# Performance work log

Measured on AMD Instinct MI355X. Metric: run time of the kernel, lower is better.

## Reference

```python
import jax, jax.numpy as jnp
import numpy as np

N_OBJ, N_REG = 4096, 8192
D_HO = D_HR = 512
GATE_W = 128
E = 131072


def setup_inputs() -> dict:
    key = jax.random.key(0)
    ks = jax.random.split(key, 10)
    s = 1.0 / np.sqrt(D_HO + D_HR)
    return {
        "feature_obj": jax.random.normal(ks[0], (N_OBJ, D_HO), jnp.float32),
        "feature_region": jax.random.normal(ks[1], (N_REG, D_HR), jnp.float32),
        # edge lists (tgt, src) equivalent to np.where(select_mat > 0)
        "r2o_tgt": jnp.sort(jax.random.randint(ks[2], (E,), 0, N_OBJ, jnp.int32)),
        "r2o_src": jax.random.randint(ks[3], (E,), 0, N_REG, jnp.int32),
        "o2r_tgt": jnp.sort(jax.random.randint(ks[4], (E,), 0, N_REG, jnp.int32)),
        "o2r_src": jax.random.randint(ks[5], (E,), 0, N_OBJ, jnp.int32),
        # attention gate Linear(dim_src+dim_tgt -> gate_width), bias=True
        "gw_r2o": jax.random.uniform(ks[6], (GATE_W, D_HR + D_HO), jnp.float32, -s, s),
        "gb_r2o": jnp.zeros((GATE_W,), jnp.float32),
        "gw_o2r": jax.random.uniform(ks[7], (GATE_W, D_HO + D_HR), jnp.float32, -s, s),
        "gb_o2r": jnp.zeros((GATE_W,), jnp.float32),
        # transform Sequential(ReLU, Linear(dim -> dim, bias=True))
        "tw_r2o": jax.random.uniform(ks[8], (D_HO, D_HR), jnp.float32, -s, s),
        "tb_r2o": jnp.zeros((D_HO,), jnp.float32),
        "tw_o2r": jax.random.uniform(ks[9], (D_HR, D_HO), jnp.float32, -s, s),
        "tb_o2r": jnp.zeros((D_HR,), jnp.float32),
    }


def _message(tgt_feat, src_feat, tgt_idx, src_idx, gw, gb, num_tgt):
    # gather per-edge source/target features: [E, ds], [E, dt]
    src = src_feat[src_idx]
    tgt = tgt_feat[tgt_idx]
    # Attention_Module: gate = mean(sigmoid(W @ relu(cat(src, tgt)) + b))
    g = jax.nn.relu(jnp.concatenate([src, tgt], axis=-1))
    gate = jnp.mean(jax.nn.sigmoid(g @ gw.T + gb), axis=-1, keepdims=True)  # [E, 1]
    msg = src * gate
    agg = jax.ops.segment_sum(msg, tgt_idx, num_segments=num_tgt)
    # mps_use_average=True -> per-target mean; targets with no edges stay zero
    cnt = jax.ops.segment_sum(jnp.ones((tgt_idx.shape[0], 1), msg.dtype), tgt_idx, num_segments=num_tgt)
    return agg / jnp.maximum(cnt, 1.0)


def reference(feature_obj, feature_region, r2o_tgt, r2o_src, o2r_tgt, o2r_src,
              gw_r2o, gb_r2o, gw_o2r, gb_o2r, tw_r2o, tb_r2o, tw_o2r, tb_o2r):
    m_r2o = _message(feature_obj, feature_region, r2o_tgt, r2o_src, gw_r2o, gb_r2o, N_OBJ)
    out_obj = feature_obj + jax.nn.relu(m_r2o) @ tw_r2o.T + tb_r2o
    m_o2r = _message(feature_region, feature_obj, o2r_tgt, o2r_src, gw_o2r, gb_o2r, N_REG)
    out_reg = feature_region + jax.nn.relu(m_o2r) @ tw_o2r.T + tb_o2r
    return (out_obj, out_reg)
```

## Files before the change

kernel.cpp:

```cpp
#include <hip/hip_runtime.h>

constexpr int N_OBJ = 4096, N_REG = 8192, D = 512, GW = 128, NE = 131072;

typedef __attribute__((ext_vector_type(8))) short short8;
typedef __attribute__((ext_vector_type(4))) float f32x4;
typedef __attribute__((ext_vector_type(2))) float f32x2;

__device__ inline short f2bf(float f) {
  unsigned u = __builtin_bit_cast(unsigned, f);
  unsigned r = (u + 0x7FFF + ((u >> 16) & 1)) >> 16;
  return (short)r;
}

__global__ __launch_bounds__(256) void cast_csr(
    const float* __restrict__ feat_reg, const float* __restrict__ feat_obj,
    const float* __restrict__ gw_r2o, const float* __restrict__ gw_o2r,
    const float* __restrict__ tw_r2o, const float* __restrict__ tw_o2r,
    const int* __restrict__ t_r2o, const int* __restrict__ t_o2r,
    unsigned char* __restrict__ raw_reg, short* __restrict__ relu_reg,
    unsigned char* __restrict__ raw_obj, short* __restrict__ relu_obj,
    short* __restrict__ Wreg, short* __restrict__ Wobj,
    short* __restrict__ btw_r2o, short* __restrict__ btw_o2r,
    int* __restrict__ off_r2o, int* __restrict__ off_o2r) {
  int i = blockIdx.x * 256 + threadIdx.x;
  if (i >= 1769472) {
    i -= 1769472;
    const int* tgt; int* off; int t;
    if (i <= N_OBJ) { tgt = t_r2o; off = off_r2o; t = i; }
    else {
      i -= N_OBJ + 1;
      if (i > N_REG) return;
      tgt = t_o2r; off = off_o2r; t = i;
    }
    int lo = 0, hi = NE;
    while (lo < hi) {
      int mid = (lo + hi) >> 1;
      if (tgt[mid] < t) lo = mid + 1; else hi = mid;
    }
    off[t] = lo;
    return;
  }
  if (i < 1572864) {
    const float* src; unsigned char* draw; short* drelu; int j = i;
    if (j < 1048576) { src = feat_reg; draw = raw_reg; drelu = relu_reg; }
    else { j -= 1048576; src = feat_obj; draw = raw_obj; drelu = relu_obj; }
    float4 v = ((const float4*)src)[j];
    int p = __builtin_amdgcn_cvt_pk_fp8_f32(v.x, v.y, 0, false);
    p = __builtin_amdgcn_cvt_pk_fp8_f32(v.z, v.w, p, true);
    ((unsigned*)draw)[j] = (unsigned)p;
    ((short4*)drelu)[j] = make_short4(f2bf(fmaxf(v.x, 0.f)), f2bf(fmaxf(v.y, 0.f)),
                                      f2bf(fmaxf(v.z, 0.f)), f2bf(fmaxf(v.w, 0.f)));
    return;
  }
  i -= 1572864;
  const float* src; short* dst; int di;
  if (i < 32768) {
    int row = i >> 7, c4 = i & 127;
    src = (row < 128) ? gw_r2o + (size_t)row * 1024 + c4 * 4
                      : gw_o2r + (size_t)(row - 128) * 1024 + 512 + c4 * 4;
    dst = Wreg; di = i;
  } else if (i < 65536) {
    int k = i - 32768, row = k >> 7, c4 = k & 127;
    src = (row < 128) ? gw_r2o + (size_t)row * 1024 + 512 + c4 * 4
                      : gw_o2r + (size_t)(row - 128) * 1024 + c4 * 4;
    dst = Wobj; di = k;
  } else if (i < 131072) { di = i - 65536; src = tw_r2o + (size_t)di * 4; dst = btw_r2o; }
  else                   { di = i - 131072; src = tw_o2r + (size_t)di * 4; dst = btw_o2r; }
  float4 v = *(const float4*)src;
  ((short4*)dst)[di] = make_short4(f2bf(v.x), f2bf(v.y), f2bf(v.z), f2bf(v.w));
}

struct GemmPair {
  const short* A[2]; const short* B[2];
  const float* res[2]; const float* bias[2];
  void* C[2];
  int nb0;
  int nxb;
  int ldc;
};

template<bool EPI, int BN>
__global__ __launch_bounds__(256) void gemm_pair(GemmPair gp) {
  constexpr int NF = BN / 32;
  __shared__ short As[2][128 * 32];
  __shared__ short Bs[2][BN * 32];
  int b = blockIdx.x;
  const int pi = (b >= gp.nb0) ? 1 : 0;
  if (pi) b -= gp.nb0;
  const int bx = b % gp.nxb, by = b / gp.nxb;
  const short* __restrict__ A = gp.A[pi];
  const short* __restrict__ B = gp.B[pi];
  const int ldc = gp.ldc;
  const int tid = threadIdx.x;
  const int lane = tid & 63, w = tid >> 6;
  const int m0 = by * 128, n0 = bx * BN;
  const int wm = (w >> 1) * 64, wn = (w & 1) * (BN / 2);
  const int sr = lane >> 2, sc = (lane & 3) * 8;
  const int fr = lane & 15, fk = (lane >> 4) * 8;

  f32x4 acc[4][NF];
#pragma unroll
  for (int i = 0; i < 4; ++i)
#pragma unroll
    for (int j = 0; j < NF; ++j) acc[i][j] = (f32x4){0.f, 0.f, 0.f, 0.f};

  auto stage = [&](int buf, int k0) {
#pragma unroll
    for (int h = 0; h < 2; ++h) {
      int rg = w * 32 + h * 16;
      const short* ga = A + (size_t)(m0 + rg + sr) * 512 + k0 + sc;
      __builtin_amdgcn_global_load_lds(
          (const __attribute__((address_space(1))) void*)ga,
          (__attribute__((address_space(3))) void*)&As[buf][rg * 32], 16, 0, 0);
    }
#pragma unroll
    for (int h = 0; h < BN / 64; ++h) {
      int rg = w * (BN / 4) + h * 16;
      const short* gb = B + (size_t)(n0 + rg + sr) * 512 + k0 + sc;
      __builtin_amdgcn_global_load_lds(
          (const __attribute__((address_space(1))) void*)gb,
          (__attribute__((address_space(3))) void*)&Bs[buf][rg * 32], 16, 0, 0);
    }
  };
  auto compute = [&](int buf) {
    short8 a[4], bb[NF];
#pragma unroll
    for (int i = 0; i < 4; ++i)
      a[i] = *(const short8*)&As[buf][(wm + i * 16 + fr) * 32 + fk];
#pragma unroll
    for (int j = 0; j < NF; ++j)
      bb[j] = *(const short8*)&Bs[buf][(wn + j * 16 + fr) * 32 + fk];
#pragma unroll
    for (int i = 0; i < 4; ++i)
#pragma unroll
      for (int j = 0; j < NF; ++j)
        acc[i][j] = __builtin_amdgcn_mfma_f32_16x16x32_bf16(a[i], bb[j], acc[i][j], 0, 0, 0);
  };

  stage(0, 0);
  __syncthreads();
  int cur = 0;
  for (int k0 = 0; k0 < 512 - 32; k0 += 32) {
    stage(cur ^ 1, k0 + 32);
    compute(cur);
    __syncthreads();
    cur ^= 1;
  }
  compute(cur);

  if (EPI) {
    float* C = (float*)gp.C[pi];
    const float* res = gp.res[pi];
    const float* bias = gp.bias[pi];
#pragma unroll
    for (int i = 0; i < 4; ++i)
#pragma unroll
      for (int j = 0; j < NF; ++j) {
        int n = n0 + wn + j * 16 + fr;
#pragma unroll
        for (int r = 0; r < 4; ++r) {
          int m = m0 + wm + i * 16 + (lane >> 4) * 4 + r;
          C[(size_t)m * ldc + n] = acc[i][j][r] + res[(size_t)m * ldc + n] + bias[n];
        }
      }
  } else {
    unsigned char* C = (unsigned char*)gp.C[pi];
#pragma unroll
    for (int i = 0; i < 4; ++i)
#pragma unroll
      for (int j = 0; j < NF; ++j) {
        int n = n0 + wn + j * 16 + fr;
#pragma unroll
        for (int r = 0; r < 4; ++r) {
          int m = m0 + wm + i * 16 + (lane >> 4) * 4 + r;
          int pk = __builtin_amdgcn_cvt_pk_fp8_f32(acc[i][j][r], acc[i][j][r], 0, false);
          C[(size_t)m * ldc + n] = (unsigned char)(pk & 0xFF);
        }
      }
  }
}

__global__ __launch_bounds__(256) void fused_msg(
    const unsigned char* __restrict__ Preg, const unsigned char* __restrict__ Pobj,
    const unsigned char* __restrict__ raw_reg, const unsigned char* __restrict__ raw_obj,
    const int* __restrict__ r2o_src, const int* __restrict__ o2r_src,
    const int* __restrict__ off_r2o, const int* __restrict__ off_o2r,
    const float* __restrict__ gb_r2o, const float* __restrict__ gb_o2r,
    short* __restrict__ m_obj, short* __restrict__ m_reg) {
  __shared__ float red[4][512];
  int t = blockIdx.x;
  const unsigned char *PA, *PB, *feat; const int *src, *off; const float* gb;
  short* mo; int po;
  if (t < N_OBJ) {
    PA = Preg; PB = Pobj; feat = raw_reg; src = r2o_src; off = off_r2o;
    gb = gb_r2o; mo = m_obj; po = 0;
  } else {
    t -= N_OBJ;
    PA = Pobj; PB = Preg; feat = raw_obj; src = o2r_src; off = off_o2r;
    gb = gb_o2r; mo = m_reg; po = 128;
  }
  const int tid = threadIdx.x, lane = tid & 63, w = tid >> 6;
  const int hw = lane >> 5, l = lane & 31;
  const int e0 = off[t], e1 = off[t + 1];
  unsigned pbu = *(const unsigned*)&PB[(size_t)t * 256 + po + l * 4];
  f32x2 pb01 = __builtin_amdgcn_cvt_pk_f32_fp8((int)pbu, false);
  f32x2 pb23 = __builtin_amdgcn_cvt_pk_f32_fp8((int)pbu, true);
  float4 gbv = *(const float4*)&gb[l * 4];
  const float c0 = pb01.x + gbv.x, c1 = pb01.y + gbv.y;
  const float c2 = pb23.x + gbv.z, c3 = pb23.y + gbv.w;
  float acc[16] = {};

  auto sig4 = [&](unsigned pau) -> float {
    f32x2 a01 = __builtin_amdgcn_cvt_pk_f32_fp8((int)pau, false);
    f32x2 a23 = __builtin_amdgcn_cvt_pk_f32_fp8((int)pau, true);
    return __builtin_amdgcn_rcpf(1.f + __expf(-(a01.x + c0)))
         + __builtin_amdgcn_rcpf(1.f + __expf(-(a01.y + c1)))
         + __builtin_amdgcn_rcpf(1.f + __expf(-(a23.x + c2)))
         + __builtin_amdgcn_rcpf(1.f + __expf(-(a23.y + c3)));
  };
  auto accum = [&](uint4 fv, float gs) {
    f32x2 f0 = __builtin_amdgcn_cvt_pk_f32_fp8((int)fv.x, false);
    f32x2 f1 = __builtin_amdgcn_cvt_pk_f32_fp8((int)fv.x, true);
    f32x2 f2 = __builtin_amdgcn_cvt_pk_f32_fp8((int)fv.y, false);
    f32x2 f3 = __builtin_amdgcn_cvt_pk_f32_fp8((int)fv.y, true);
    f32x2 f4 = __builtin_amdgcn_cvt_pk_f32_fp8((int)fv.z, false);
    f32x2 f5 = __builtin_amdgcn_cvt_pk_f32_fp8((int)fv.z, true);
    f32x2 f6 = __builtin_amdgcn_cvt_pk_f32_fp8((int)fv.w, false);
    f32x2 f7 = __builtin_amdgcn_cvt_pk_f32_fp8((int)fv.w, true);
    acc[0]  += f0.x * gs; acc[1]  += f0.y * gs;
    acc[2]  += f1.x * gs; acc[3]  += f1.y * gs;
    acc[4]  += f2.x * gs; acc[5]  += f2.y * gs;
    acc[6]  += f3.x * gs; acc[7]  += f3.y * gs;
    acc[8]  += f4.x * gs; acc[9]  += f4.y * gs;
    acc[10] += f5.x * gs; acc[11] += f5.y * gs;
    acc[12] += f6.x * gs; acc[13] += f6.y * gs;
    acc[14] += f7.x * gs; acc[15] += f7.y * gs;
  };

  int e = e0 + w * 2 + hw;
  for (; e + 8 < e1; e += 16) {
    int s0 = src[e], s1 = src[e + 8];
    unsigned pau0 = *(const unsigned*)&PA[(size_t)s0 * 256 + po + l * 4];
    uint4 fv0 = *(const uint4*)&feat[(size_t)s0 * 512 + l * 16];
    unsigned pau1 = *(const unsigned*)&PA[(size_t)s1 * 256 + po + l * 4];
    uint4 fv1 = *(const uint4*)&feat[(size_t)s1 * 512 + l * 16];
    float gs0 = sig4(pau0), gs1 = sig4(pau1);
#pragma unroll
    for (int msk = 16; msk >= 1; msk >>= 1) {
      gs0 += __shfl_xor(gs0, msk, 64);
      gs1 += __shfl_xor(gs1, msk, 64);
    }
    accum(fv0, gs0);
    accum(fv1, gs1);
  }
  for (; e < e1; e += 8) {
    int s = src[e];
    unsigned pau = *(const unsigned*)&PA[(size_t)s * 256 + po + l * 4];
    uint4 fv = *(const uint4*)&feat[(size_t)s * 512 + l * 16];
    float gs = sig4(pau);
#pragma unroll
    for (int msk = 16; msk >= 1; msk >>= 1) gs += __shfl_xor(gs, msk, 64);
    accum(fv, gs);
  }
#pragma unroll
  for (int jj = 0; jj < 16; ++jj) acc[jj] += __shfl_xor(acc[jj], 32, 64);
  if (hw == 0) {
#pragma unroll
    for (int q = 0; q < 4; ++q)
      *(float4*)&red[w][l * 16 + q * 4] =
          (float4){acc[q * 4], acc[q * 4 + 1], acc[q * 4 + 2], acc[q * 4 + 3]};
  }
  __syncthreads();
  const float inv = (1.0f / 128.0f) / fmaxf((float)(e1 - e0), 1.0f);
  const int d = tid * 2;
  float s0 = red[0][d] + red[1][d] + red[2][d] + red[3][d];
  float s1 = red[0][d + 1] + red[1][d + 1] + red[2][d + 1] + red[3][d + 1];
  short2 o;
  o.x = f2bf(fmaxf(s0 * inv, 0.f));
  o.y = f2bf(fmaxf(s1 * inv, 0.f));
  *(short2*)(mo + (size_t)t * 512 + d) = o;
}

extern "C" void kernel_launch(void* const* d_in, const int* in_sizes, int n_in,
                              void* d_out, int out_size, void* d_ws, size_t ws_size,
                              hipStream_t stream) {
  const float* feat_obj = (const float*)d_in[0];
  const float* feat_reg = (const float*)d_in[1];
  const int*   r2o_tgt  = (const int*)d_in[2];
  const int*   r2o_src  = (const int*)d_in[3];
  const int*   o2r_tgt  = (const int*)d_in[4];
  const int*   o2r_src  = (const int*)d_in[5];
  const float* gw_r2o   = (const float*)d_in[6];
  const float* gb_r2o   = (const float*)d_in[7];
  const float* gw_o2r   = (const float*)d_in[8];
  const float* gb_o2r   = (const float*)d_in[9];
  const float* tw_r2o   = (const float*)d_in[10];
  const float* tb_r2o   = (const float*)d_in[11];
  const float* tw_o2r   = (const float*)d_in[12];
  const float* tb_o2r   = (const float*)d_in[13];
  float* out_obj = (float*)d_out;
  float* out_reg = out_obj + (size_t)N_OBJ * D;

  size_t cur = 0;
  auto alloc = [&](size_t bytes) -> void* {
    cur = (cur + 255) & ~(size_t)255;
    void* p = (char*)d_ws + cur;
    cur += bytes;
    return p;
  };
  int*   off_r2o = (int*)alloc((N_OBJ + 1) * sizeof(int));
  int*   off_o2r = (int*)alloc((N_REG + 1) * sizeof(int));
  unsigned char* raw_reg = (unsigned char*)alloc((size_t)N_REG * D);
  unsigned char* raw_obj = (unsigned char*)alloc((size_t)N_OBJ * D);
  short* relu_reg= (short*)alloc((size_t)N_REG * D * 2);
  short* relu_obj= (short*)alloc((size_t)N_OBJ * D * 2);
  short* Wreg    = (short*)alloc((size_t)256 * D * 2);
  short* Wobj    = (short*)alloc((size_t)256 * D * 2);
  short* btw_r2o = (short*)alloc((size_t)D * D * 2);
  short* btw_o2r = (short*)alloc((size_t)D * D * 2);
  unsigned char* Preg = (unsigned char*)alloc((size_t)N_REG * 256);
  unsigned char* Pobj = (unsigned char*)alloc((size_t)N_OBJ * 256);
  short* m_obj   = (short*)alloc((size_t)N_OBJ * D * 2);
  short* m_reg   = (short*)alloc((size_t)N_REG * D * 2);

  cast_csr<<<6961, 256, 0, stream>>>(feat_reg, feat_obj, gw_r2o, gw_o2r, tw_r2o, tw_o2r,
                                     r2o_tgt, o2r_tgt,
                                     raw_reg, relu_reg, raw_obj, relu_obj,
                                     Wreg, Wobj, btw_r2o, btw_o2r, off_r2o, off_o2r);

  GemmPair proj;
  proj.A[0] = relu_reg; proj.B[0] = Wreg; proj.C[0] = Preg;
  proj.A[1] = relu_obj; proj.B[1] = Wobj; proj.C[1] = Pobj;
  proj.res[0] = proj.res[1] = nullptr; proj.bias[0] = proj.bias[1] = nullptr;
  proj.nb0 = 4 * (N_REG / 128); proj.nxb = 4; proj.ldc = 256;
  gemm_pair<false, 64><<<384, 256, 0, stream>>>(proj);

  fused_msg<<<N_OBJ + N_REG, 256, 0, stream>>>(Preg, Pobj, raw_reg, raw_obj,
                                               r2o_src, o2r_src, off_r2o, off_o2r,
                                               gb_r2o, gb_o2r, m_obj, m_reg);

  GemmPair tr;
  tr.A[0] = m_reg; tr.B[0] = btw_o2r; tr.res[0] = feat_reg; tr.bias[0] = tb_o2r; tr.C[0] = out_reg;
  tr.A[1] = m_obj; tr.B[1] = btw_r2o; tr.res[1] = feat_obj; tr.bias[1] = tb_r2o; tr.C[1] = out_obj;
  tr.nb0 = 4 * (N_REG / 128); tr.nxb = 4; tr.ldc = D;
  gemm_pair<true, 128><<<384, 256, 0, stream>>>(tr);
}
```

Before: 188.6 us.

## Map one wavefront per target node in fused message kernel, drop LDS reduction

Reworks fused_msg so that each 64-lane wavefront owns one target node instead of a 256-thread block per node. Lanes are split into four quarter-wave groups of 16, each handling one edge at a time with 8 gate columns and 32 feature bytes per lane. The per-block shared-memory reduction and __syncthreads are replaced by cross-quarter shuffles, and the output is written as a single 16-byte store per lane. This cuts block count and sync overhead, at the cost of more registers per lane (32 accumulators) and less edge-level parallelism per target, since only 4 edges are in flight per node instead of 8.

```diff
diff --git a/kernel.cpp b/kernel.cpp
--- a/kernel.cpp
+++ b/kernel.cpp
@@ -187,8 +187,9 @@
     const int* __restrict__ off_r2o, const int* __restrict__ off_o2r,
     const float* __restrict__ gb_r2o, const float* __restrict__ gb_o2r,
     short* __restrict__ m_obj, short* __restrict__ m_reg) {
-  __shared__ float red[4][512];
-  int t = blockIdx.x;
+  const int tid = threadIdx.x, w = tid >> 6, lane = tid & 63;
+  const int q = lane >> 4, l = lane & 15;
+  int t = blockIdx.x * 4 + w;
   const unsigned char *PA, *PB, *feat; const int *src, *off; const float* gb;
   short* mo; int po;
   if (t < N_OBJ) {
@@ -199,86 +200,60 @@
     PA = Pobj; PB = Preg; feat = raw_obj; src = o2r_src; off = off_o2r;
     gb = gb_o2r; mo = m_reg; po = 128;
   }
-  const int tid = threadIdx.x, lane = tid & 63, w = tid >> 6;
-  const int hw = lane >> 5, l = lane & 31;
   const int e0 = off[t], e1 = off[t + 1];
-  unsigned pbu = *(const unsigned*)&PB[(size_t)t * 256 + po + l * 4];
-  f32x2 pb01 = __builtin_amdgcn_cvt_pk_f32_fp8((int)pbu, false);
-  f32x2 pb23 = __builtin_amdgcn_cvt_pk_f32_fp8((int)pbu, true);
-  float4 gbv = *(const float4*)&gb[l * 4];
-  const float c0 = pb01.x + gbv.x, c1 = pb01.y + gbv.y;
-  const float c2 = pb23.x + gbv.z, c3 = pb23.y + gbv.w;
-  float acc[16] = {};
-
-  auto sig4 = [&](unsigned pau) -> float {
-    f32x2 a01 = __builtin_amdgcn_cvt_pk_f32_fp8((int)pau, false);
-    f32x2 a23 = __builtin_amdgcn_cvt_pk_f32_fp8((int)pau, true);
-    return __builtin_amdgcn_rcpf(1.f + __expf(-(a01.x + c0)))
-         + __builtin_amdgcn_rcpf(1.f + __expf(-(a01.y + c1)))
-         + __builtin_amdgcn_rcpf(1.f + __expf(-(a23.x + c2)))
-         + __builtin_amdgcn_rcpf(1.f + __expf(-(a23.y + c3)));
-  };
-  auto accum = [&](uint4 fv, float gs) {
-    f32x2 f0 = __builtin_amdgcn_cvt_pk_f32_fp8((int)fv.x, false);
-    f32x2 f1 = __builtin_amdgcn_cvt_pk_f32_fp8((int)fv.x, true);
-    f32x2 f2 = __builtin_amdgcn_cvt_pk_f32_fp8((int)fv.y, false);
-    f32x2 f3 = __builtin_amdgcn_cvt_pk_f32_fp8((int)fv.y, true);
-    f32x2 f4 = __builtin_amdgcn_cvt_pk_f32_fp8((int)fv.z, false);
-    f32x2 f5 = __builtin_amdgcn_cvt_pk_f32_fp8((int)fv.z, true);
-    f32x2 f6 = __builtin_amdgcn_cvt_pk_f32_fp8((int)fv.w, false);
-    f32x2 f7 = __builtin_amdgcn_cvt_pk_f32_fp8((int)fv.w, true);
-    acc[0]  += f0.x * gs; acc[1]  += f0.y * gs;
-    acc[2]  += f1.x * gs; acc[3]  += f1.y * gs;
-    acc[4]  += f2.x * gs; acc[5]  += f2.y * gs;
-    acc[6]  += f3.x * gs; acc[7]  += f3.y * gs;
-    acc[8]  += f4.x * gs; acc[9]  += f4.y * gs;
-    acc[10] += f5.x * gs; acc[11] += f5.y * gs;
-    acc[12] += f6.x * gs; acc[13] += f6.y * gs;
-    acc[14] += f7.x * gs; acc[15] += f7.y * gs;
-  };
-
-  int e = e0 + w * 2 + hw;
-  for (; e + 8 < e1; e += 16) {
-    int s0 = src[e], s1 = src[e + 8];
-    unsigned pau0 = *(const unsigned*)&PA[(size_t)s0 * 256 + po + l * 4];
-    uint4 fv0 = *(const uint4*)&feat[(size_t)s0 * 512 + l * 16];
-    unsigned pau1 = *(const unsigned*)&PA[(size_t)s1 * 256 + po + l * 4];
-    uint4 fv1 = *(const uint4*)&feat[(size_t)s1 * 512 + l * 16];
-    float gs0 = sig4(pau0), gs1 = sig4(pau1);
-#pragma unroll
-    for (int msk = 16; msk >= 1; msk >>= 1) {
-      gs0 += __shfl_xor(gs0, msk, 64);
-      gs1 += __shfl_xor(gs1, msk, 64);
-    }
-    accum(fv0, gs0);
-    accum(fv1, gs1);
-  }
-  for (; e < e1; e += 8) {
+  uint2 pbu = *(const uint2*)&PB[(size_t)t * 256 + po + l * 8];
+  f32x2 pb0 = __builtin_amdgcn_cvt_pk_f32_fp8((int)pbu.x, false);
+  f32x2 pb1 = __builtin_amdgcn_cvt_pk_f32_fp8((int)pbu.x, true);
+  f32x2 pb2 = __builtin_amdgcn_cvt_pk_f32_fp8((int)pbu.y, false);
+  f32x2 pb3 = __builtin_amdgcn_cvt_pk_f32_fp8((int)pbu.y, true);
+  float4 gA = *(const float4*)&gb[l * 8];
+  float4 gB = *(const float4*)&gb[l * 8 + 4];
+  const float c0 = pb0.x + gA.x, c1 = pb0.y + gA.y;
+  const float c2 = pb1.x + gA.z, c3 = pb1.y + gA.w;
+  const float c4 = pb2.x + gB.x, c5 = pb2.y + gB.y;
+  const float c6 = pb3.x + gB.z, c7 = pb3.y + gB.w;
+
+  float acc[32] = {};
+  for (int e = e0 + q; e < e1; e += 4) {
     int s = src[e];
-    unsigned pau = *(const unsigned*)&PA[(size_t)s * 256 + po + l * 4];
-    uint4 fv = *(const uint4*)&feat[(size_t)s * 512 + l * 16];
-    float gs = sig4(pau);
-#pragma unroll
-    for (int msk = 16; msk >= 1; msk >>= 1) gs += __shfl_xor(gs, msk, 64);
-    accum(fv, gs);
-  }
-#pragma unroll
-  for (int jj = 0; jj < 16; ++jj) acc[jj] += __shfl_xor(acc[jj], 32, 64);
-  if (hw == 0) {
-#pragma unroll
-    for (int q = 0; q < 4; ++q)
-      *(float4*)&red[w][l * 16 + q * 4] =
-          (float4){acc[q * 4], acc[q * 4 + 1], acc[q * 4 + 2], acc[q * 4 + 3]};
-  }
-  __syncthreads();
+    uint2 pau = *(const uint2*)&PA[(size_t)s * 256 + po + l * 8];
+    uint4 f0 = *(const uint4*)&feat[(size_t)s * 512 + l * 32];
+    uint4 f1 = *(const uint4*)&feat[(size_t)s * 512 + l * 32 + 16];
+    f32x2 a0 = __builtin_amdgcn_cvt_pk_f32_fp8((int)pau.x, false);
+    f32x2 a1 = __builtin_amdgcn_cvt_pk_f32_fp8((int)pau.x, true);
+    f32x2 a2 = __builtin_amdgcn_cvt_pk_f32_fp8((int)pau.y, false);
+    f32x2 a3 = __builtin_amdgcn_cvt_pk_f32_fp8((int)pau.y, true);
+    float gs = __builtin_amdgcn_rcpf(1.f + __expf(-(a0.x + c0)))
+             + __builtin_amdgcn_rcpf(1.f + __expf(-(a0.y + c1)))
+             + __builtin_amdgcn_rcpf(1.f + __expf(-(a1.x + c2)))
+             + __builtin_amdgcn_rcpf(1.f + __expf(-(a1.y + c3)))
+             + __builtin_amdgcn_rcpf(1.f + __expf(-(a2.x + c4)))
+             + __builtin_amdgcn_rcpf(1.f + __expf(-(a2.y + c5)))
+             + __builtin_amdgcn_rcpf(1.f + __expf(-(a3.x + c6)))
+             + __builtin_amdgcn_rcpf(1.f + __expf(-(a3.y + c7)));
+#pragma unroll
+    for (int msk = 8; msk >= 1; msk >>= 1) gs += __shfl_xor(gs, msk, 64);
+    unsigned fd[8] = {f0.x, f0.y, f0.z, f0.w, f1.x, f1.y, f1.z, f1.w};
+#pragma unroll
+    for (int d = 0; d < 8; ++d) {
+      f32x2 lo = __builtin_amdgcn_cvt_pk_f32_fp8((int)fd[d], false);
+      f32x2 hi = __builtin_amdgcn_cvt_pk_f32_fp8((int)fd[d], true);
+      acc[d * 4 + 0] += lo.x * gs;
+      acc[d * 4 + 1] += lo.y * gs;
+      acc[d * 4 + 2] += hi.x * gs;
+      acc[d * 4 + 3] += hi.y * gs;
+    }
+  }
+#pragma unroll
+  for (int j = 0; j < 32; ++j) {
+    acc[j] += __shfl_xor(acc[j], 16, 64);
+    acc[j] += __shfl_xor(acc[j], 32, 64);
+  }
   const float inv = (1.0f / 128.0f) / fmaxf((float)(e1 - e0), 1.0f);
-  const int d = tid * 2;
-  float s0 = red[0][d] + red[1][d] + red[2][d] + red[3][d];
-  float s1 = red[0][d + 1] + red[1][d + 1] + red[2][d + 1] + red[3][d + 1];
-  short2 o;
-  o.x = f2bf(fmaxf(s0 * inv, 0.f));
-  o.y = f2bf(fmaxf(s1 * inv, 0.f));
-  *(short2*)(mo + (size_t)t * 512 + d) = o;
+  short8 o;
+#pragma unroll
+  for (int k = 0; k < 8; ++k) o[k] = f2bf(fmaxf(acc[q * 8 + k] * inv, 0.f));
+  *(short8*)(mo + (size_t)t * 512 + l * 32 + q * 8) = o;
 }
 
 extern "C" void kernel_launch(void* const* d_in, const int* in_sizes, int n_in,
@@ -335,9 +310,9 @@
   proj.nb0 = 4 * (N_REG / 128); proj.nxb = 4; proj.ldc = 256;
   gemm_pair<false, 64><<<384, 256, 0, stream>>>(proj);
 
-  fused_msg<<<N_OBJ + N_REG, 256, 0, stream>>>(Preg, Pobj, raw_reg, raw_obj,
-                                               r2o_src, o2r_src, off_r2o, off_o2r,
-                                               gb_r2o, gb_o2r, m_obj, m_reg);
+  fused_msg<<<(N_OBJ + N_REG) / 4, 256, 0, stream>>>(Preg, Pobj, raw_reg, raw_obj,
+                                                     r2o_src, o2r_src, off_r2o, off_o2r,
+                                                     gb_r2o, gb_o2r, m_obj, m_reg);
 
   GemmPair tr;
   tr.A[0] = m_reg; tr.B[0] = btw_o2r; tr.res[0] = feat_reg; tr.bias[0] = tb_o2r; tr.C[0] = out_reg;
```

New measurement: 193.3 us. 1.02x slower.

## Interleave per-node gate projection and fp8 features into one gathered record

Applied to the files above, without the earlier changes.

Packs each source node's 128-byte fp8 gate projection next to its 512-byte fp8 features in a 640-byte record, so each edge gather reads one contiguous record instead of two separate arrays. The projection GEMM epilogue now splits its output columns between these records and a separate compact target-side projection array. The message kernel's two-edge unrolled loop is also dropped in favour of a simple single-edge loop, which may reduce memory-level parallelism per wave.

```diff
diff --git a/kernel.cpp b/kernel.cpp
--- a/kernel.cpp
+++ b/kernel.cpp
@@ -1,6 +1,7 @@
 #include <hip/hip_runtime.h>
 
 constexpr int N_OBJ = 4096, N_REG = 8192, D = 512, GW = 128, NE = 131072;
+constexpr int REC = 640;
 
 typedef __attribute__((ext_vector_type(8))) short short8;
 typedef __attribute__((ext_vector_type(4))) float f32x4;
@@ -17,8 +18,8 @@
     const float* __restrict__ gw_r2o, const float* __restrict__ gw_o2r,
     const float* __restrict__ tw_r2o, const float* __restrict__ tw_o2r,
     const int* __restrict__ t_r2o, const int* __restrict__ t_o2r,
-    unsigned char* __restrict__ raw_reg, short* __restrict__ relu_reg,
-    unsigned char* __restrict__ raw_obj, short* __restrict__ relu_obj,
+    unsigned char* __restrict__ comb_reg, short* __restrict__ relu_reg,
+    unsigned char* __restrict__ comb_obj, short* __restrict__ relu_obj,
     short* __restrict__ Wreg, short* __restrict__ Wobj,
     short* __restrict__ btw_r2o, short* __restrict__ btw_o2r,
     int* __restrict__ off_r2o, int* __restrict__ off_o2r) {
@@ -41,13 +42,14 @@
     return;
   }
   if (i < 1572864) {
-    const float* src; unsigned char* draw; short* drelu; int j = i;
-    if (j < 1048576) { src = feat_reg; draw = raw_reg; drelu = relu_reg; }
-    else { j -= 1048576; src = feat_obj; draw = raw_obj; drelu = relu_obj; }
+    const float* src; unsigned char* comb; short* drelu; int j = i;
+    if (j < 1048576) { src = feat_reg; comb = comb_reg; drelu = relu_reg; }
+    else { j -= 1048576; src = feat_obj; comb = comb_obj; drelu = relu_obj; }
     float4 v = ((const float4*)src)[j];
     int p = __builtin_amdgcn_cvt_pk_fp8_f32(v.x, v.y, 0, false);
     p = __builtin_amdgcn_cvt_pk_fp8_f32(v.z, v.w, p, true);
-    ((unsigned*)draw)[j] = (unsigned)p;
+    int row = j >> 7, c4 = j & 127;
+    *(unsigned*)&comb[(size_t)row * REC + 128 + c4 * 4] = (unsigned)p;
     ((short4*)drelu)[j] = make_short4(f2bf(fmaxf(v.x, 0.f)), f2bf(fmaxf(v.y, 0.f)),
                                       f2bf(fmaxf(v.z, 0.f)), f2bf(fmaxf(v.w, 0.f)));
     return;
@@ -74,9 +76,9 @@
   const short* A[2]; const short* B[2];
   const float* res[2]; const float* bias[2];
   void* C[2];
-  int nb0;
-  int nxb;
-  int ldc;
+  void* Clo[2]; void* Chi[2];
+  int lo_stride[2]; int hi_stride[2];
+  int nb0, nxb, ldc;
 };
 
 template<bool EPI, int BN>
@@ -90,7 +92,6 @@
   const int bx = b % gp.nxb, by = b / gp.nxb;
   const short* __restrict__ A = gp.A[pi];
   const short* __restrict__ B = gp.B[pi];
-  const int ldc = gp.ldc;
   const int tid = threadIdx.x;
   const int lane = tid & 63, w = tid >> 6;
   const int m0 = by * 128, n0 = bx * BN;
@@ -152,6 +153,7 @@
     float* C = (float*)gp.C[pi];
     const float* res = gp.res[pi];
     const float* bias = gp.bias[pi];
+    const int ldc = gp.ldc;
 #pragma unroll
     for (int i = 0; i < 4; ++i)
 #pragma unroll
@@ -164,7 +166,9 @@
         }
       }
   } else {
-    unsigned char* C = (unsigned char*)gp.C[pi];
+    unsigned char* Clo = (unsigned char*)gp.Clo[pi];
+    unsigned char* Chi = (unsigned char*)gp.Chi[pi];
+    const int ls = gp.lo_stride[pi], hs = gp.hi_stride[pi];
 #pragma unroll
     for (int i = 0; i < 4; ++i)
 #pragma unroll
@@ -174,35 +178,36 @@
         for (int r = 0; r < 4; ++r) {
           int m = m0 + wm + i * 16 + (lane >> 4) * 4 + r;
           int pk = __builtin_amdgcn_cvt_pk_fp8_f32(acc[i][j][r], acc[i][j][r], 0, false);
-          C[(size_t)m * ldc + n] = (unsigned char)(pk & 0xFF);
+          unsigned char v = (unsigned char)(pk & 0xFF);
+          if (n < 128) Clo[(size_t)m * ls + n] = v;
+          else         Chi[(size_t)m * hs + (n - 128)] = v;
         }
       }
   }
 }
 
 __global__ __launch_bounds__(256) void fused_msg(
-    const unsigned char* __restrict__ Preg, const unsigned char* __restrict__ Pobj,
-    const unsigned char* __restrict__ raw_reg, const unsigned char* __restrict__ raw_obj,
+    const unsigned char* __restrict__ comb_reg, const unsigned char* __restrict__ comb_obj,
+    const unsigned char* __restrict__ PB_r2o, const unsigned char* __restrict__ PB_o2r,
     const int* __restrict__ r2o_src, const int* __restrict__ o2r_src,
     const int* __restrict__ off_r2o, const int* __restrict__ off_o2r,
     const float* __restrict__ gb_r2o, const float* __restrict__ gb_o2r,
     short* __restrict__ m_obj, short* __restrict__ m_reg) {
   __shared__ float red[4][512];
   int t = blockIdx.x;
-  const unsigned char *PA, *PB, *feat; const int *src, *off; const float* gb;
-  short* mo; int po;
+  const unsigned char *recs, *PBp; const int *src, *off; const float* gb; short* mo;
   if (t < N_OBJ) {
-    PA = Preg; PB = Pobj; feat = raw_reg; src = r2o_src; off = off_r2o;
-    gb = gb_r2o; mo = m_obj; po = 0;
+    recs = comb_reg; PBp = PB_r2o; src = r2o_src; off = off_r2o;
+    gb = gb_r2o; mo = m_obj;
   } else {
     t -= N_OBJ;
-    PA = Pobj; PB = Preg; feat = raw_obj; src = o2r_src; off = off_o2r;
-    gb = gb_o2r; mo = m_reg; po = 128;
+    recs = comb_obj; PBp = PB_o2r; src = o2r_src; off = off_o2r;
+    gb = gb_o2r; mo = m_reg;
   }
   const int tid = threadIdx.x, lane = tid & 63, w = tid >> 6;
   const int hw = lane >> 5, l = lane & 31;
   const int e0 = off[t], e1 = off[t + 1];
-  unsigned pbu = *(const unsigned*)&PB[(size_t)t * 256 + po + l * 4];
+  unsigned pbu = *(const unsigned*)&PBp[(size_t)t * 128 + l * 4];
   f32x2 pb01 = __builtin_amdgcn_cvt_pk_f32_fp8((int)pbu, false);
   f32x2 pb23 = __builtin_amdgcn_cvt_pk_f32_fp8((int)pbu, true);
   float4 gbv = *(const float4*)&gb[l * 4];
@@ -210,57 +215,29 @@
   const float c2 = pb23.x + gbv.z, c3 = pb23.y + gbv.w;
   float acc[16] = {};
 
-  auto sig4 = [&](unsigned pau) -> float {
+  for (int e = e0 + w * 2 + hw; e < e1; e += 8) {
+    int s = src[e];
+    const unsigned char* rec = recs + (size_t)s * REC;
+    unsigned pau = *(const unsigned*)&rec[l * 4];
+    uint4 fv = *(const uint4*)&rec[128 + l * 16];
     f32x2 a01 = __builtin_amdgcn_cvt_pk_f32_fp8((int)pau, false);
     f32x2 a23 = __builtin_amdgcn_cvt_pk_f32_fp8((int)pau, true);
-    return __builtin_amdgcn_rcpf(1.f + __expf(-(a01.x + c0)))
-         + __builtin_amdgcn_rcpf(1.f + __expf(-(a01.y + c1)))
-         + __builtin_amdgcn_rcpf(1.f + __expf(-(a23.x + c2)))
-         + __builtin_amdgcn_rcpf(1.f + __expf(-(a23.y + c3)));
-  };
-  auto accum = [&](uint4 fv, float gs) {
-    f32x2 f0 = __builtin_amdgcn_cvt_pk_f32_fp8((int)fv.x, false);
-    f32x2 f1 = __builtin_amdgcn_cvt_pk_f32_fp8((int)fv.x, true);
-    f32x2 f2 = __builtin_amdgcn_cvt_pk_f32_fp8((int)fv.y, false);
-    f32x2 f3 = __builtin_amdgcn_cvt_pk_f32_fp8((int)fv.y, true);
-    f32x2 f4 = __builtin_amdgcn_cvt_pk_f32_fp8((int)fv.z, false);
-    f32x2 f5 = __builtin_amdgcn_cvt_pk_f32_fp8((int)fv.z, true);
-    f32x2 f6 = __builtin_amdgcn_cvt_pk_f32_fp8((int)fv.w, false);
-    f32x2 f7 = __builtin_amdgcn_cvt_pk_f32_fp8((int)fv.w, true);
-    acc[0]  += f0.x * gs; acc[1]  += f0.y * gs;
-    acc[2]  += f1.x * gs; acc[3]  += f1.y * gs;
-    acc[4]  += f2.x * gs; acc[5]  += f2.y * gs;
-    acc[6]  += f3.x * gs; acc[7]  += f3.y * gs;
-    acc[8]  += f4.x * gs; acc[9]  += f4.y * gs;
-    acc[10] += f5.x * gs; acc[11] += f5.y * gs;
-    acc[12] += f6.x * gs; acc[13] += f6.y * gs;
-    acc[14] += f7.x * gs; acc[15] += f7.y * gs;
-  };
-
-  int e = e0 + w * 2 + hw;
-  for (; e + 8 < e1; e += 16) {
-    int s0 = src[e], s1 = src[e + 8];
-    unsigned pau0 = *(const unsigned*)&PA[(size_t)s0 * 256 + po + l * 4];
-    uint4 fv0 = *(const uint4*)&feat[(size_t)s0 * 512 + l * 16];
-    unsigned pau1 = *(const unsigned*)&PA[(size_t)s1 * 256 + po + l * 4];
-    uint4 fv1 = *(const uint4*)&feat[(size_t)s1 * 512 + l * 16];
-    float gs0 = sig4(pau0), gs1 = sig4(pau1);
-#pragma unroll
-    for (int msk = 16; msk >= 1; msk >>= 1) {
-      gs0 += __shfl_xor(gs0, msk, 64);
-      gs1 += __shfl_xor(gs1, msk, 64);
-    }
-    accum(fv0, gs0);
-    accum(fv1, gs1);
-  }
-  for (; e < e1; e += 8) {
-    int s = src[e];
-    unsigned pau = *(const unsigned*)&PA[(size_t)s * 256 + po + l * 4];
-    uint4 fv = *(const uint4*)&feat[(size_t)s * 512 + l * 16];
-    float gs = sig4(pau);
+    float gs = __builtin_amdgcn_rcpf(1.f + __expf(-(a01.x + c0)))
+             + __builtin_amdgcn_rcpf(1.f + __expf(-(a01.y + c1)))
+             + __builtin_amdgcn_rcpf(1.f + __expf(-(a23.x + c2)))
+             + __builtin_amdgcn_rcpf(1.f + __expf(-(a23.y + c3)));
 #pragma unroll
     for (int msk = 16; msk >= 1; msk >>= 1) gs += __shfl_xor(gs, msk, 64);
-    accum(fv, gs);
+    unsigned fd[4] = {fv.x, fv.y, fv.z, fv.w};
+#pragma unroll
+    for (int d = 0; d < 4; ++d) {
+      f32x2 lo = __builtin_amdgcn_cvt_pk_f32_fp8((int)fd[d], false);
+      f32x2 hi = __builtin_amdgcn_cvt_pk_f32_fp8((int)fd[d], true);
+      acc[d * 4 + 0] += lo.x * gs;
+      acc[d * 4 + 1] += lo.y * gs;
+      acc[d * 4 + 2] += hi.x * gs;
+      acc[d * 4 + 3] += hi.y * gs;
+    }
   }
 #pragma unroll
   for (int jj = 0; jj < 16; ++jj) acc[jj] += __shfl_xor(acc[jj], 32, 64);
@@ -310,38 +287,45 @@
   };
   int*   off_r2o = (int*)alloc((N_OBJ + 1) * sizeof(int));
   int*   off_o2r = (int*)alloc((N_REG + 1) * sizeof(int));
-  unsigned char* raw_reg = (unsigned char*)alloc((size_t)N_REG * D);
-  unsigned char* raw_obj = (unsigned char*)alloc((size_t)N_OBJ * D);
+  unsigned char* comb_reg = (unsigned char*)alloc((size_t)N_REG * REC);
+  unsigned char* comb_obj = (unsigned char*)alloc((size_t)N_OBJ * REC);
+  unsigned char* PB_r2o   = (unsigned char*)alloc((size_t)N_OBJ * 128);
+  unsigned char* PB_o2r   = (unsigned char*)alloc((size_t)N_REG * 128);
   short* relu_reg= (short*)alloc((size_t)N_REG * D * 2);
   short* relu_obj= (short*)alloc((size_t)N_OBJ * D * 2);
   short* Wreg    = (short*)alloc((size_t)256 * D * 2);
   short* Wobj    = (short*)alloc((size_t)256 * D * 2);
   short* btw_r2o = (short*)alloc((size_t)D * D * 2);
   short* btw_o2r = (short*)alloc((size_t)D * D * 2);
-  unsigned char* Preg = (unsigned char*)alloc((size_t)N_REG * 256);
-  unsigned char* Pobj = (unsigned char*)alloc((size_t)N_OBJ * 256);
   short* m_obj   = (short*)alloc((size_t)N_OBJ * D * 2);
   short* m_reg   = (short*)alloc((size_t)N_REG * D * 2);
 
   cast_csr<<<6961, 256, 0, stream>>>(feat_reg, feat_obj, gw_r2o, gw_o2r, tw_r2o, tw_o2r,
                                      r2o_tgt, o2r_tgt,
-                                     raw_reg, relu_reg, raw_obj, relu_obj,
+                                     comb_reg, relu_reg, comb_obj, relu_obj,
                                      Wreg, Wobj, btw_r2o, btw_o2r, off_r2o, off_o2r);
 
   GemmPair proj;
-  proj.A[0] = relu_reg; proj.B[0] = Wreg; proj.C[0] = Preg;
-  proj.A[1] = relu_obj; proj.B[1] = Wobj; proj.C[1] = Pobj;
+  proj.A[0] = relu_reg; proj.B[0] = Wreg;
+  proj.A[1] = relu_obj; proj.B[1] = Wobj;
+  proj.Clo[0] = comb_reg; proj.lo_stride[0] = REC;
+  proj.Chi[0] = PB_o2r;   proj.hi_stride[0] = 128;
+  proj.Clo[1] = PB_r2o;   proj.lo_stride[1] = 128;
+  proj.Chi[1] = comb_obj; proj.hi_stride[1] = REC;
+  proj.C[0] = proj.C[1] = nullptr;
   proj.res[0] = proj.res[1] = nullptr; proj.bias[0] = proj.bias[1] = nullptr;
   proj.nb0 = 4 * (N_REG / 128); proj.nxb = 4; proj.ldc = 256;
   gemm_pair<false, 64><<<384, 256, 0, stream>>>(proj);
 
-  fused_msg<<<N_OBJ + N_REG, 256, 0, stream>>>(Preg, Pobj, raw_reg, raw_obj,
+  fused_msg<<<N_OBJ + N_REG, 256, 0, stream>>>(comb_reg, comb_obj, PB_r2o, PB_o2r,
                                                r2o_src, o2r_src, off_r2o, off_o2r,
                                                gb_r2o, gb_o2r, m_obj, m_reg);
 
   GemmPair tr;
   tr.A[0] = m_reg; tr.B[0] = btw_o2r; tr.res[0] = feat_reg; tr.bias[0] = tb_o2r; tr.C[0] = out_reg;
   tr.A[1] = m_obj; tr.B[1] = btw_r2o; tr.res[1] = feat_obj; tr.bias[1] = tb_r2o; tr.C[1] = out_obj;
+  tr.Clo[0] = tr.Clo[1] = tr.Chi[0] = tr.Chi[1] = nullptr;
+  tr.lo_stride[0] = tr.lo_stride[1] = tr.hi_stride[0] = tr.hi_stride[1] = 0;
   tr.nb0 = 4 * (N_REG / 128); tr.nxb = 4; tr.ldc = D;
   gemm_pair<true, 128><<<384, 256, 0, stream>>>(tr);
 }
```

Measured after the change: 189.8 us. No clear change (+0.6%).
